# Performance work log

Hardware: AMD Instinct MI355X
Metric: run time of the kernel (lower is better)

The kernel has to match this reference:

```python
import jax, jax.numpy as jnp
import numpy as np

N_POINTS, N_GRIDS, K = 1024, 512, 7


def setup_inputs() -> dict:
    key = jax.random.key(0)
    k1, k2, k3, k4 = jax.random.split(key, 4)
    points = jax.random.uniform(k1, (N_POINTS, 3), dtype=jnp.float32) * 2.0 - 1.0
    volume_centers = jax.random.uniform(k2, (N_GRIDS, 3), dtype=jnp.float32) * 2.0 - 1.0
    min_s, max_s = 0.01, 1.0
    scales = jax.random.uniform(k3, (N_GRIDS,), dtype=jnp.float32) * (max_s - min_s) + min_s
    mosaic_sdf_values = jax.random.normal(k4, (N_GRIDS, K, K, K), dtype=jnp.float32)
    return {"points": points, "volume_centers": volume_centers,
            "scales": scales, "mosaic_sdf_values": mosaic_sdf_values}


def reference(points, volume_centers, scales, mosaic_sdf_values):
    G, k = mosaic_sdf_values.shape[0], mosaic_sdf_values.shape[1]
    # scaled relative positions: (N, G, 3)
    rel = (points[:, None, :] - volume_centers[None, :, :]) / scales[None, :, None]
    # grid node coordinates in [0,1]^3, flattened: (k^3, 3)
    lin = jnp.linspace(0.0, 1.0, k, dtype=points.dtype)
    gx, gy, gz = jnp.meshgrid(lin, lin, lin, indexing='ij')
    coords = jnp.stack([gx, gy, gz], axis=-1).reshape(-1, 3)
    # squared distance ||rel - coord||^2 expanded -> avoids (N,G,k^3,3) materialization
    d2 = (jnp.sum(rel * rel, axis=-1)[..., None]
          - 2.0 * jnp.einsum('ngd,cd->ngc', rel, coords)
          + jnp.sum(coords * coords, axis=-1)[None, None, :])  # (N, G, k^3)
    dist = jnp.sqrt(jnp.maximum(d2, 0.0))
    # original: weight = dist where dist <= 1 else 0, normalized over grid nodes
    w = jnp.where(dist <= 1.0, dist, 0.0)
    s = jnp.sum(w, axis=-1, keepdims=True)
    w = jnp.where(s > 0, w / jnp.where(s == 0, 1.0, s), 0.0)  # nan_to_num(0) equivalent
    vals = mosaic_sdf_values.reshape(G, -1)  # (G, k^3)
    interp = jnp.einsum('ngc,gc->ng', w, vals)  # (N, G)
    # per-grid blend weight: relu(1 - ||rel||), normalized over grids
    pdist = jnp.linalg.norm(rel, axis=-1)  # (N, G)
    gw = jax.nn.relu(1.0 - pdist)
    gs = jnp.sum(gw, axis=-1, keepdims=True)
    gw = jnp.where(gs > 0, gw / jnp.where(gs == 0, 1.0, gs), 0.0)
    return jnp.sum(interp * gw, axis=-1)  # (N,)
```

## Files before the change

kernel.cpp:

```cpp
#include <hip/hip_runtime.h>


#define NPTS   1024
#define NGRIDS 512
#define TPB    512
#define NBLK   512
#define STEP   (1.0f / 6.0f)
#define FSQRT(x) __builtin_amdgcn_sqrtf(x)

__global__ __launch_bounds__(TPB, 4) void msdf_fused(
    const float* __restrict__ points,
    const float* __restrict__ centers,
    const float* __restrict__ scales,
    const float* __restrict__ vals,
    float* __restrict__ out)
{
    __shared__ float4 s_pair[8][128];
    __shared__ unsigned short s_gid[8][128];
    __shared__ int   s_c[8];
    __shared__ float s_d[8];
    __shared__ float s_red[8][2];

    const int bid  = blockIdx.x;
    const int t    = threadIdx.x;
    const int w    = t >> 6;
    const int lane = t & 63;
    const int grp  = t >> 4;
    const int sub  = t & 15;

    const int   n  = (bid << 1) + (w >> 2);
    const float px = points[n * 3 + 0];
    const float py = points[n * 3 + 1];
    const float pz = points[n * 3 + 2];

    float dsum  = 0.0f;
    int   cbase = 0;
    #pragma unroll
    for (int r = 0; r < 2; ++r) {
        const int g = ((w & 3) << 7) + (r << 6) + lane;
        const float invs = 1.0f / scales[g];
        const float rx = (px - centers[g * 3 + 0]) * invs;
        const float ry = (py - centers[g * 3 + 1]) * invs;
        const float rz = (pz - centers[g * 3 + 2]) * invs;
        const float gwr = 1.0f - FSQRT(rx * rx + ry * ry + rz * rz);
        const bool  act = (gwr > 0.0f);
        const unsigned long long m = __ballot(act);
        if (act) {
            const int pos = cbase + (int)__popcll(m & ((1ull << lane) - 1ull));
            s_pair[w][pos] = make_float4(rx, ry, rz, gwr);
            s_gid[w][pos]  = (unsigned short)g;
            dsum += gwr;
        }
        cbase += (int)__popcll(m);
    }
    #pragma unroll
    for (int o = 32; o >= 1; o >>= 1) dsum += __shfl_xor(dsum, o);
    if (lane == 0) { s_c[w] = cbase; s_d[w] = dsum; }
    __syncthreads();

    const int o1 = s_c[0];
    const int o2 = o1 + s_c[1];
    const int o3 = o2 + s_c[2];
    const int o4 = o3 + s_c[3];
    const int o5 = o4 + s_c[4];
    const int o6 = o5 + s_c[5];
    const int o7 = o6 + s_c[6];
    const int CT = o7 + s_c[7];
    const float den0 = s_d[0] + s_d[1] + s_d[2] + s_d[3];
    const float den1 = s_d[4] + s_d[5] + s_d[6] + s_d[7];

    float acc0 = 0.0f, acc1 = 0.0f;
    for (int a = grp; a < CT; a += 32) {
        const int seg = (a >= o1) + (a >= o2) + (a >= o3) + (a >= o4)
                      + (a >= o5) + (a >= o6) + (a >= o7);
        const int b0  = (seg == 0) ? 0 : (seg == 1) ? o1
                      : (seg == 2) ? o2 : (seg == 3) ? o3
                      : (seg == 4) ? o4 : (seg == 5) ? o5
                      : (seg == 6) ? o6 : o7;
        const float4 pr  = s_pair[seg][a - b0];
        const int    gid = (int)s_gid[seg][a - b0];
        const float* __restrict__ grow = vals + gid * 343;

        float dz2[7];
        #pragma unroll
        for (int l = 0; l < 7; ++l) { const float d = pr.z - l * STEP; dz2[l] = d * d; }

        float ws = 0.0f, vs = 0.0f;
        #pragma unroll
        for (int rr = 0; rr < 3; ++rr) {
            const int rowid = sub + (rr << 4);
            const int i = (rowid * 9363) >> 16;
            const int j = rowid - i * 7;
            const float dxv = pr.x - (float)i * STEP;
            const float dyv = pr.y - (float)j * STEP;
            const float dxy = dxv * dxv + dyv * dyv;
            const float* __restrict__ vr = grow + rowid * 7;
            #pragma unroll
            for (int l = 0; l < 7; ++l) {
                const float d2 = dxy + dz2[l];
                const float wt = (d2 <= 1.0f) ? FSQRT(d2) : 0.0f;
                ws += wt;
                vs  = fmaf(wt, vr[l], vs);
            }
        }
        if (sub < 7) {
            const float dxv = pr.x - 1.0f;
            const float dyv = pr.y - 1.0f;
            const float dzv = pr.z - (float)sub * STEP;
            const float d2  = dxv * dxv + dyv * dyv + dzv * dzv;
            const float wt  = (d2 <= 1.0f) ? FSQRT(d2) : 0.0f;
            ws += wt;
            vs  = fmaf(wt, grow[336 + sub], vs);
        }
        #pragma unroll
        for (int o = 8; o >= 1; o >>= 1) {
            ws += __shfl_xor(ws, o);
            vs += __shfl_xor(vs, o);
        }
        const float interp = (ws > 0.0f) ? (vs / ws) : 0.0f;
        if (sub == 0) {
            const float contrib = interp * pr.w;
            if (seg < 4) acc0 += contrib;
            else         acc1 += contrib;
        }
    }

    #pragma unroll
    for (int o = 32; o >= 1; o >>= 1) {
        acc0 += __shfl_xor(acc0, o);
        acc1 += __shfl_xor(acc1, o);
    }
    if (lane == 0) { s_red[w][0] = acc0; s_red[w][1] = acc1; }
    __syncthreads();
    if (t < 2) {
        float nm = 0.0f;
        #pragma unroll
        for (int i = 0; i < 8; ++i) nm += s_red[i][t];
        const float dn = (t == 0) ? den0 : den1;
        out[(bid << 1) + t] = (dn > 0.0f) ? (nm / dn) : 0.0f;
    }
}

extern "C" void kernel_launch(void* const* d_in, const int* in_sizes, int n_in,
                              void* d_out, int out_size, void* d_ws, size_t ws_size,
                              hipStream_t stream) {
    const float* points  = (const float*)d_in[0];
    const float* centers = (const float*)d_in[1];
    const float* scales  = (const float*)d_in[2];
    const float* vals    = (const float*)d_in[3];
    float* out = (float*)d_out;

    msdf_fused<<<NBLK, TPB, 0, stream>>>(points, centers, scales, vals, out);
}
```

Measured before the change: 14.19 us.

## Assign one point per block instead of two, doubling grid size

Each 512-thread block now handles a single point, with each of 8 waves screening 64 grids, instead of two points per block with each wave covering 128 grids. This doubles the number of blocks and gives each block roughly half the active (point, grid) pairs. The aim is more parallelism and shorter per-block tails on a GPU with many CUs. The cost is that block setup, barriers and scale/center loads are repeated twice as often.

Result: slower. 14.93 us (+5.2%).

```diff
diff --git a/kernel.cpp b/kernel.cpp
--- a/kernel.cpp
+++ b/kernel.cpp
@@ -4,7 +4,7 @@
 #define NPTS   1024
 #define NGRIDS 512
 #define TPB    512
-#define NBLK   512
+#define NBLK   1024
 #define STEP   (1.0f / 6.0f)
 #define FSQRT(x) __builtin_amdgcn_sqrtf(x)
 
@@ -15,11 +15,11 @@
     const float* __restrict__ vals,
     float* __restrict__ out)
 {
-    __shared__ float4 s_pair[8][128];
-    __shared__ unsigned short s_gid[8][128];
+    __shared__ float4 s_pair[8][64];
+    __shared__ unsigned short s_gid[8][64];
     __shared__ int   s_c[8];
     __shared__ float s_d[8];
-    __shared__ float s_red[8][2];
+    __shared__ float s_red[8];
 
     const int bid  = blockIdx.x;
     const int t    = threadIdx.x;
@@ -28,16 +28,12 @@
     const int grp  = t >> 4;
     const int sub  = t & 15;
 
-    const int   n  = (bid << 1) + (w >> 2);
-    const float px = points[n * 3 + 0];
-    const float py = points[n * 3 + 1];
-    const float pz = points[n * 3 + 2];
+    const float px = points[bid * 3 + 0];
+    const float py = points[bid * 3 + 1];
+    const float pz = points[bid * 3 + 2];
 
-    float dsum  = 0.0f;
-    int   cbase = 0;
-    #pragma unroll
-    for (int r = 0; r < 2; ++r) {
-        const int g = ((w & 3) << 7) + (r << 6) + lane;
+    {
+        const int g = (w << 6) + lane;
         const float invs = 1.0f / scales[g];
         const float rx = (px - centers[g * 3 + 0]) * invs;
         const float ry = (py - centers[g * 3 + 1]) * invs;
@@ -46,16 +42,15 @@
         const bool  act = (gwr > 0.0f);
         const unsigned long long m = __ballot(act);
         if (act) {
-            const int pos = cbase + (int)__popcll(m & ((1ull << lane) - 1ull));
+            const int pos = (int)__popcll(m & ((1ull << lane) - 1ull));
             s_pair[w][pos] = make_float4(rx, ry, rz, gwr);
             s_gid[w][pos]  = (unsigned short)g;
-            dsum += gwr;
         }
-        cbase += (int)__popcll(m);
+        float dsum = act ? gwr : 0.0f;
+        #pragma unroll
+        for (int o = 32; o >= 1; o >>= 1) dsum += __shfl_xor(dsum, o);
+        if (lane == 0) { s_c[w] = (int)__popcll(m); s_d[w] = dsum; }
     }
-    #pragma unroll
-    for (int o = 32; o >= 1; o >>= 1) dsum += __shfl_xor(dsum, o);
-    if (lane == 0) { s_c[w] = cbase; s_d[w] = dsum; }
     __syncthreads();
 
     const int o1 = s_c[0];
@@ -65,12 +60,12 @@
     const int o5 = o4 + s_c[4];
     const int o6 = o5 + s_c[5];
     const int o7 = o6 + s_c[6];
-    const int CT = o7 + s_c[7];
-    const float den0 = s_d[0] + s_d[1] + s_d[2] + s_d[3];
-    const float den1 = s_d[4] + s_d[5] + s_d[6] + s_d[7];
+    const int C  = o7 + s_c[7];
+    const float den = s_d[0] + s_d[1] + s_d[2] + s_d[3]
+                    + s_d[4] + s_d[5] + s_d[6] + s_d[7];
 
-    float acc0 = 0.0f, acc1 = 0.0f;
-    for (int a = grp; a < CT; a += 32) {
+    float acc = 0.0f;
+    for (int a = grp; a < C; a += 32) {
         const int seg = (a >= o1) + (a >= o2) + (a >= o3) + (a >= o4)
                       + (a >= o5) + (a >= o6) + (a >= o7);
         const int b0  = (seg == 0) ? 0 : (seg == 1) ? o1
@@ -118,26 +113,17 @@
             vs += __shfl_xor(vs, o);
         }
         const float interp = (ws > 0.0f) ? (vs / ws) : 0.0f;
-        if (sub == 0) {
-            const float contrib = interp * pr.w;
-            if (seg < 4) acc0 += contrib;
-            else         acc1 += contrib;
-        }
+        if (sub == 0) acc += interp * pr.w;
     }
 
     #pragma unroll
-    for (int o = 32; o >= 1; o >>= 1) {
-        acc0 += __shfl_xor(acc0, o);
-        acc1 += __shfl_xor(acc1, o);
-    }
-    if (lane == 0) { s_red[w][0] = acc0; s_red[w][1] = acc1; }
+    for (int o = 32; o >= 1; o >>= 1) acc += __shfl_xor(acc, o);
+    if (lane == 0) s_red[w] = acc;
     __syncthreads();
-    if (t < 2) {
-        float nm = 0.0f;
-        #pragma unroll
-        for (int i = 0; i < 8; ++i) nm += s_red[i][t];
-        const float dn = (t == 0) ? den0 : den1;
-        out[(bid << 1) + t] = (dn > 0.0f) ? (nm / dn) : 0.0f;
+    if (t == 0) {
+        const float nm = s_red[0] + s_red[1] + s_red[2] + s_red[3]
+                       + s_red[4] + s_red[5] + s_red[6] + s_red[7];
+        out[bid] = (den > 0.0f) ? (nm / den) : 0.0f;
     }
 }
 
```

## Use 32-lane groups per grid with precomputed per-thread node coordinates

Applied to the files above, without the earlier changes.

Each active (point, grid) pair is now handled by 32 lanes instead of 16. Each lane covers 11 strided grid nodes, and their coordinates and flat indices are computed once into registers before the loop. This replaces the row/column decomposition and the separate tail for the last row. Global loads become coalesced across lanes, and the leftover-node branch disappears. In exchange each pair gets fewer per-lane iterations but one extra shuffle reduction step, and the register arrays raise register use.

Result: slower. 18.26 us (+28.7%).

```diff
diff --git a/kernel.cpp b/kernel.cpp
--- a/kernel.cpp
+++ b/kernel.cpp
@@ -25,8 +25,8 @@
     const int t    = threadIdx.x;
     const int w    = t >> 6;
     const int lane = t & 63;
-    const int grp  = t >> 4;
-    const int sub  = t & 15;
+    const int grp  = t >> 5;
+    const int sub  = t & 31;
 
     const int   n  = (bid << 1) + (w >> 2);
     const float px = points[n * 3 + 0];
@@ -69,8 +69,25 @@
     const float den0 = s_d[0] + s_d[1] + s_d[2] + s_d[3];
     const float den1 = s_d[4] + s_d[5] + s_d[6] + s_d[7];
 
+    float CX[11], CY[11], CZ[11];
+    int   CA[11];
+    #pragma unroll
+    for (int k = 0; k < 11; ++k) {
+        const int c     = sub + (k << 5);
+        const bool okc  = (c <= 342);
+        const int  cc   = okc ? c : 342;
+        const int  i    = (cc * 1338) >> 16;
+        const int  rem  = cc - i * 49;
+        const int  j    = (rem * 9363) >> 16;
+        const int  l    = rem - j * 7;
+        CX[k] = okc ? (float)i * STEP : 99.0f;
+        CY[k] = okc ? (float)j * STEP : 99.0f;
+        CZ[k] = okc ? (float)l * STEP : 99.0f;
+        CA[k] = cc;
+    }
+
     float acc0 = 0.0f, acc1 = 0.0f;
-    for (int a = grp; a < CT; a += 32) {
+    for (int a = grp; a < CT; a += 16) {
         const int seg = (a >= o1) + (a >= o2) + (a >= o3) + (a >= o4)
                       + (a >= o5) + (a >= o6) + (a >= o7);
         const int b0  = (seg == 0) ? 0 : (seg == 1) ? o1
@@ -81,39 +98,20 @@
         const int    gid = (int)s_gid[seg][a - b0];
         const float* __restrict__ grow = vals + gid * 343;
 
-        float dz2[7];
-        #pragma unroll
-        for (int l = 0; l < 7; ++l) { const float d = pr.z - l * STEP; dz2[l] = d * d; }
-
         float ws = 0.0f, vs = 0.0f;
         #pragma unroll
-        for (int rr = 0; rr < 3; ++rr) {
-            const int rowid = sub + (rr << 4);
-            const int i = (rowid * 9363) >> 16;
-            const int j = rowid - i * 7;
-            const float dxv = pr.x - (float)i * STEP;
-            const float dyv = pr.y - (float)j * STEP;
-            const float dxy = dxv * dxv + dyv * dyv;
-            const float* __restrict__ vr = grow + rowid * 7;
-            #pragma unroll
-            for (int l = 0; l < 7; ++l) {
-                const float d2 = dxy + dz2[l];
-                const float wt = (d2 <= 1.0f) ? FSQRT(d2) : 0.0f;
-                ws += wt;
-                vs  = fmaf(wt, vr[l], vs);
-            }
-        }
-        if (sub < 7) {
-            const float dxv = pr.x - 1.0f;
-            const float dyv = pr.y - 1.0f;
-            const float dzv = pr.z - (float)sub * STEP;
-            const float d2  = dxv * dxv + dyv * dyv + dzv * dzv;
-            const float wt  = (d2 <= 1.0f) ? FSQRT(d2) : 0.0f;
+        for (int k = 0; k < 11; ++k) {
+            const float v  = grow[CA[k]];
+            const float dx = pr.x - CX[k];
+            const float dy = pr.y - CY[k];
+            const float dz = pr.z - CZ[k];
+            const float d2 = fmaf(dx, dx, fmaf(dy, dy, dz * dz));
+            const float wt = (d2 <= 1.0f) ? FSQRT(d2) : 0.0f;
             ws += wt;
-            vs  = fmaf(wt, grow[336 + sub], vs);
+            vs  = fmaf(wt, v, vs);
         }
         #pragma unroll
-        for (int o = 8; o >= 1; o >>= 1) {
+        for (int o = 16; o >= 1; o >>= 1) {
             ws += __shfl_xor(ws, o);
             vs += __shfl_xor(vs, o);
         }
```
